# Performance work log

Hardware: AMD Instinct MI355X
Metric: run time of the kernel (lower is better)

## Reference

```python
import jax, jax.numpy as jnp
import numpy as np

B, L, Q = 2, 512, 512
E, W, D, H_NLM = 1024, 1024, 8, 32
NH = 16
HD = E // NH
SA, SO = 512, 1024
V = 8192
T = 6  # max_thought_step
SYN_H = 2048


def setup_inputs() -> dict:
    key = jax.random.key(0)
    ks = jax.random.split(key, 24)
    n = lambda k, shp, s=0.02: jax.random.normal(k, shp, dtype=jnp.float32) * s
    return {
        "x": jax.random.randint(ks[0], (B, L), 0, V),
        "num_output_q": Q,
        "emb": n(ks[1], (V, E)),
        "w_kv": n(ks[2], (E, E)),
        "w_q_sync": n(ks[3], (SA, E)),
        "wq": n(ks[4], (E, E)),
        "wk": n(ks[5], (E, E)),
        "wv": n(ks[6], (E, E)),
        "wo": n(ks[7], (E, E)),
        "ws1": n(ks[8], (E + W, SYN_H)),
        "bs1": jnp.zeros((SYN_H,), jnp.float32),
        "ws2": n(ks[9], (SYN_H, W)),
        "bs2": jnp.zeros((W,), jnp.float32),
        "nlm_w1": n(ks[10], (W, D, H_NLM), 0.1),
        "nlm_b1": jnp.zeros((W, H_NLM), jnp.float32),
        "nlm_w2": n(ks[11], (W, H_NLM), 0.1),
        "nlm_b2": jnp.zeros((W,), jnp.float32),
        "out_w": n(ks[12], (SO, V)),
        "out_b": jnp.zeros((V,), jnp.float32),
        "z_init": jax.random.normal(ks[13], (W,), dtype=jnp.float32),
        "pah_init": jax.random.normal(ks[14], (W, D), dtype=jnp.float32),
        "decay_a": jnp.zeros((SA,), jnp.float32),
        "decay_o": jnp.zeros((SO,), jnp.float32),
        "idx_la": jax.random.randint(ks[15], (SA,), 0, W),
        "idx_ra": jax.random.randint(ks[16], (SA,), 0, W),
        "idx_lo": jax.random.randint(ks[17], (SO,), 0, W),
        "idx_ro": jax.random.randint(ks[18], (SO,), 0, W),
    }


def _rope(xh, pos):
    # xh: [B, NH, S, HD]; rotate-half RoPE
    half = HD // 2
    inv = 1.0 / (10000.0 ** (jnp.arange(half, dtype=jnp.float32) / half))
    ang = pos.astype(jnp.float32)[:, None] * inv[None, :]  # [S, half]
    cos, sin = jnp.cos(ang), jnp.sin(ang)
    x1, x2 = xh[..., :half], xh[..., half:]
    return jnp.concatenate([x1 * cos - x2 * sin, x2 * cos + x1 * sin], axis=-1)


def _attention(q_in, kv, wq, wk, wv, wo):
    # causal cross-attention with RoPE on q and k
    Bq, Sq, _ = q_in.shape
    Sk = kv.shape[1]
    heads = lambda t: t.reshape(t.shape[0], t.shape[1], NH, HD).transpose(0, 2, 1, 3)
    qh = _rope(heads(q_in @ wq), jnp.arange(Sq))
    kh = _rope(heads(kv @ wk), jnp.arange(Sk))
    vh = heads(kv @ wv)
    scores = jnp.einsum('bhqd,bhkd->bhqk', qh, kh) / jnp.sqrt(jnp.float32(HD))
    i = jnp.arange(Sq)[:, None]
    j = jnp.arange(Sk)[None, :]
    scores = jnp.where(j <= i + (Sk - Sq), scores, jnp.float32(-1e30))
    out = jnp.einsum('bhqk,bhkd->bhqd', jax.nn.softmax(scores, axis=-1), vh)
    return out.transpose(0, 2, 1, 3).reshape(Bq, Sq, E) @ wo


def _compute_sync(hist, idx_l, idx_r, decay):
    # hist: list of [B,Q,W]; exponentially-decayed gather-multiply-reduce over time
    seq = jnp.stack(hist, axis=1)  # [B, Tn, Q, W]
    Tn = seq.shape[1]
    t_back = jnp.arange(Tn - 1, -1, -1, dtype=jnp.float32).reshape(1, Tn, 1, 1)
    ed = jnp.exp(-t_back * decay.reshape(1, 1, 1, -1))  # [1,Tn,1,S]
    sm = seq[..., idx_l] * ed * seq[..., idx_r]  # [B,Tn,Q,S]
    return sm.sum(axis=1) / jnp.sqrt(ed.sum(axis=1))  # [B,Q,S]


def reference(x, num_output_q, emb, w_kv, w_q_sync, wq, wk, wv, wo, ws1, bs1, ws2, bs2,
              nlm_w1, nlm_b1, nlm_w2, nlm_b2, out_w, out_b, z_init, pah_init,
              decay_a, decay_o, idx_la, idx_ra, idx_lo, idx_ro):
    emb_input = emb[x]                      # [B,L,E]
    kv = emb_input @ w_kv                   # [B,L,E]
    pah = jnp.broadcast_to(pah_init, (B, Q, W, D))
    z = jnp.broadcast_to(z_init, (B, Q, W))
    hist = [z]
    sync_a = _compute_sync(hist, idx_la, idx_ra, decay_a)
    outs = []
    for _ in range(T):
        q = sync_a @ w_q_sync               # [B,Q,E]
        attn_out = _attention(q, kv, wq, wk, wv, wo)
        pre = jnp.concatenate([attn_out, z], axis=-1)        # [B,Q,E+W]
        pre = jax.nn.gelu(pre @ ws1 + bs1) @ ws2 + bs2        # synapse -> [B,Q,W]
        pah = jnp.concatenate([pah[..., 1:], pre[..., None]], axis=-1)
        h = jax.nn.gelu(jnp.einsum('bqwd,wdh->bqwh', pah, nlm_w1) + nlm_b1)
        z = jnp.einsum('bqwh,wh->bqw', h, nlm_w2) + nlm_b2    # neuron-level model
        hist.append(z)
        sync_a = _compute_sync(hist, idx_la, idx_ra, decay_a)
        sync_o = _compute_sync(hist, idx_lo, idx_ro, decay_o)
        outs.append(sync_o @ out_w + out_b)                   # [B,Q,V]
    return jnp.stack(outs, axis=0)          # [T,B,Q,V]
```

## Files before the change

### kernel.cpp

```cpp
#include <hip/hip_runtime.h>

#define B_ 2
#define L_ 512
#define Q_ 512
#define E_ 1024
#define W_ 1024
#define D_ 8
#define H_ 32
#define NH_ 16
#define HD_ 64
#define SA_ 512
#define SO_ 1024
#define V_ 8192
#define T_ 6
#define SYNH_ 2048

#define BQ_ 1024
#define BL_ 1024

typedef __attribute__((ext_vector_type(8))) short bf16x8;
typedef __attribute__((ext_vector_type(4))) float f32x4;

__device__ __forceinline__ float gelu_f(float x) {
    const float c = 0.7978845608028654f;
    float x3 = x * x * x;
    return 0.5f * x * (1.0f + tanhf(c * (x + 0.044715f * x3)));
}

__device__ __forceinline__ unsigned short f2bf(float x) {
    unsigned int u = __float_as_uint(x);
    u += 0x7fffu + ((u >> 16) & 1u);
    return (unsigned short)(u >> 16);
}
__device__ __forceinline__ float bf2f(unsigned short h) {
    return __uint_as_float(((unsigned int)h) << 16);
}

__device__ __forceinline__ void gload16(const void* g, void* l) {
    __builtin_amdgcn_global_load_lds(
        (const __attribute__((address_space(1))) void*)g,
        (__attribute__((address_space(3))) void*)l, 16, 0, 0);
}

template<int TILE>
__global__ __launch_bounds__(256) void gemm_split_db(
    const unsigned short* __restrict__ Ah, const unsigned short* __restrict__ Al,
    const unsigned short* __restrict__ Bh, const unsigned short* __restrict__ Bl,
    float* __restrict__ C, unsigned short* __restrict__ CHp, unsigned short* __restrict__ CLp,
    int ldc, const float* __restrict__ bias,
    int M, int N, int K, int act)
{
    constexpr int FR = TILE / 32;
    constexpr int TS = TILE * 32;
    constexpr int NP = TS / 8 / 256;
    __shared__ unsigned short sAh[2][TS], sAl[2][TS], sBh[2][TS], sBl[2][TS];

    const int tid  = threadIdx.x;
    const int wave = tid >> 6;
    const int lane = tid & 63;
    const int r15 = lane & 15;
    const int r4  = lane >> 4;
    const int bm = blockIdx.y * TILE;
    const int bn = blockIdx.x * TILE;
    const int wm = (wave >> 1) * (TILE / 2);
    const int wn = (wave & 1) * (TILE / 2);

    f32x4 acc[FR][FR] = {};

    size_t goffA[NP], goffB[NP];
    int ldst[NP];
#pragma unroll
    for (int p2 = 0; p2 < NP; ++p2) {
        int ch = p2 * 256 + tid;
        int row = ch >> 2, c = ch & 3;
        int cs = c ^ ((row >> 1) & 3);
        goffA[p2] = (size_t)(bm + row) * K + cs * 8;
        goffB[p2] = (size_t)(bn + row) * K + cs * 8;
        ldst[p2] = (p2 * 256 + wave * 64) * 8;
    }

    const int nk = K / 32;
#pragma unroll
    for (int p2 = 0; p2 < NP; ++p2) {
        gload16(Ah + goffA[p2], &sAh[0][ldst[p2]]);
        gload16(Al + goffA[p2], &sAl[0][ldst[p2]]);
        gload16(Bh + goffB[p2], &sBh[0][ldst[p2]]);
        gload16(Bl + goffB[p2], &sBl[0][ldst[p2]]);
    }
    asm volatile("s_waitcnt vmcnt(0)" ::: "memory");
    __syncthreads();

    for (int t = 0; t < nk; ++t) {
        const int cur = t & 1;
        if (t + 1 < nk) {
            const size_t kadd = (size_t)(t + 1) * 32;
#pragma unroll
            for (int p2 = 0; p2 < NP; ++p2) {
                gload16(Ah + goffA[p2] + kadd, &sAh[cur ^ 1][ldst[p2]]);
                gload16(Al + goffA[p2] + kadd, &sAl[cur ^ 1][ldst[p2]]);
                gload16(Bh + goffB[p2] + kadd, &sBh[cur ^ 1][ldst[p2]]);
                gload16(Bl + goffB[p2] + kadd, &sBl[cur ^ 1][ldst[p2]]);
            }
        }
        bf16x8 afh[FR], afl[FR], bfh[FR], bfl[FR];
#pragma unroll
        for (int i = 0; i < FR; ++i) {
            const int row = wm + i * 16 + r15;
            const int off = row * 32 + (r4 ^ ((row >> 1) & 3)) * 8;
            afh[i] = *(const bf16x8*)(&sAh[cur][off]);
            afl[i] = *(const bf16x8*)(&sAl[cur][off]);
        }
#pragma unroll
        for (int j = 0; j < FR; ++j) {
            const int row = wn + j * 16 + r15;
            const int off = row * 32 + (r4 ^ ((row >> 1) & 3)) * 8;
            bfh[j] = *(const bf16x8*)(&sBh[cur][off]);
            bfl[j] = *(const bf16x8*)(&sBl[cur][off]);
        }
#pragma unroll
        for (int i = 0; i < FR; ++i)
#pragma unroll
            for (int j = 0; j < FR; ++j) {
                acc[i][j] = __builtin_amdgcn_mfma_f32_16x16x32_bf16(afh[i], bfh[j], acc[i][j], 0, 0, 0);
                acc[i][j] = __builtin_amdgcn_mfma_f32_16x16x32_bf16(afh[i], bfl[j], acc[i][j], 0, 0, 0);
                acc[i][j] = __builtin_amdgcn_mfma_f32_16x16x32_bf16(afl[i], bfh[j], acc[i][j], 0, 0, 0);
            }
        asm volatile("s_waitcnt vmcnt(0)" ::: "memory");
        __syncthreads();
    }

    const int crow0 = bm + wm + r4 * 4;
    const int ccol0 = bn + wn + r15;
#pragma unroll
    for (int i = 0; i < FR; ++i) {
#pragma unroll
        for (int j = 0; j < FR; ++j) {
            const int col = ccol0 + j * 16;
            const float bv = bias ? bias[col] : 0.0f;
#pragma unroll
            for (int r = 0; r < 4; ++r) {
                const int row = crow0 + i * 16 + r;
                float v = acc[i][j][r] + bv;
                if (act) v = gelu_f(v);
                const size_t o = (size_t)row * ldc + col;
                if (C) C[o] = v;
                if (CHp) {
                    unsigned short hh = f2bf(v);
                    CHp[o] = hh;
                    CLp[o] = f2bf(v - bf2f(hh));
                }
            }
        }
    }
}

__global__ __launch_bounds__(256) void attn_mfma(
    const unsigned short* __restrict__ qh_h, const unsigned short* __restrict__ qh_l,
    const unsigned short* __restrict__ kh_h, const unsigned short* __restrict__ kh_l,
    const unsigned short* __restrict__ vt_h, const unsigned short* __restrict__ vt_l,
    unsigned short* __restrict__ ctxH, unsigned short* __restrict__ ctxL)
{
    __shared__ unsigned short sKh[64 * 64], sKl[64 * 64];
    __shared__ unsigned short sVh[64 * 64], sVl[64 * 64];
    __shared__ unsigned short sPh[64 * 64], sPl[64 * 64];

    const int tid  = threadIdx.x;
    const int wave = tid >> 6;
    const int lane = tid & 63;
    const int r15 = lane & 15;
    const int r4  = lane >> 4;
    const int qt = blockIdx.x;
    const int h  = blockIdx.y;
    const int b  = blockIdx.z;
    const int bh = b * NH_ + h;
    const int qbase = qt * 64 + wave * 16;

    bf16x8 qa[2][2];
    {
        const unsigned short* qr_h = qh_h + ((size_t)bh * Q_ + qbase + r15) * HD_ + r4 * 8;
        const unsigned short* qr_l = qh_l + ((size_t)bh * Q_ + qbase + r15) * HD_ + r4 * 8;
        qa[0][0] = *(const bf16x8*)(qr_h);
        qa[1][0] = *(const bf16x8*)(qr_h + 32);
        qa[0][1] = *(const bf16x8*)(qr_l);
        qa[1][1] = *(const bf16x8*)(qr_l + 32);
    }

    f32x4 of[4] = {};
    float mrow[4] = {-1e30f, -1e30f, -1e30f, -1e30f};
    float lrow[4] = {};

    const int row0 = tid >> 3,        i70 = tid & 7;
    const int row1 = 32 + (tid >> 3), i71 = tid & 7;
    const int ko0 = row0 * 64 + ((i70 * 8) ^ ((row0 & 7) << 3));
    const int ko1 = row1 * 64 + ((i71 * 8) ^ ((row1 & 7) << 3));
    const size_t vo0 = (size_t)row0 * L_ + ((i70 * 8) ^ ((row0 & 7) << 3));
    const size_t vo1 = (size_t)row1 * L_ + ((i71 * 8) ^ ((row1 & 7) << 3));
    const int ld0 = wave * 512;
    const int ld1 = 2048 + wave * 512;

    const unsigned short* kb_h = kh_h + (size_t)bh * L_ * HD_;
    const unsigned short* kb_l = kh_l + (size_t)bh * L_ * HD_;
    const unsigned short* vb_h = vt_h + (size_t)bh * HD_ * L_;
    const unsigned short* vb_l = vt_l + (size_t)bh * HD_ * L_;

    for (int kt = 0; kt <= qt; ++kt) {
        gload16(kb_h + kt * 4096 + ko0, sKh + ld0);
        gload16(kb_h + kt * 4096 + ko1, sKh + ld1);
        gload16(kb_l + kt * 4096 + ko0, sKl + ld0);
        gload16(kb_l + kt * 4096 + ko1, sKl + ld1);
        gload16(vb_h + vo0 + kt * 64, sVh + ld0);
        gload16(vb_h + vo1 + kt * 64, sVh + ld1);
        gload16(vb_l + vo0 + kt * 64, sVl + ld0);
        gload16(vb_l + vo1 + kt * 64, sVl + ld1);
        asm volatile("s_waitcnt vmcnt(0)" ::: "memory");
        __syncthreads();

        f32x4 sf[4] = {};
#pragma unroll
        for (int ks = 0; ks < 2; ++ks) {
#pragma unroll
            for (int j = 0; j < 4; ++j) {
                const int kr = j * 16 + r15;
                const int off = kr * 64 + (((ks * 32 + r4 * 8)) ^ ((kr & 7) << 3));
                bf16x8 kfh = *(const bf16x8*)(sKh + off);
                bf16x8 kfl = *(const bf16x8*)(sKl + off);
                sf[j] = __builtin_amdgcn_mfma_f32_16x16x32_bf16(qa[ks][0], kfh, sf[j], 0, 0, 0);
                sf[j] = __builtin_amdgcn_mfma_f32_16x16x32_bf16(qa[ks][0], kfl, sf[j], 0, 0, 0);
                sf[j] = __builtin_amdgcn_mfma_f32_16x16x32_bf16(qa[ks][1], kfh, sf[j], 0, 0, 0);
            }
        }

        const bool diag = (kt == qt);
#pragma unroll
        for (int j = 0; j < 4; ++j)
#pragma unroll
            for (int r = 0; r < 4; ++r) {
                float s = sf[j][r] * 0.125f;
                if (diag) {
                    int kg = kt * 64 + j * 16 + r15;
                    int qg = qt * 64 + wave * 16 + r4 * 4 + r;
                    if (kg > qg) s = -1e30f;
                }
                sf[j][r] = s;
            }

        float pv[4][4];
#pragma unroll
        for (int r = 0; r < 4; ++r) {
            float mx = fmaxf(fmaxf(sf[0][r], sf[1][r]), fmaxf(sf[2][r], sf[3][r]));
#pragma unroll
            for (int d = 1; d < 16; d <<= 1) mx = fmaxf(mx, __shfl_xor(mx, d, 64));
            float mnew = fmaxf(mrow[r], mx);
            float corr = expf(mrow[r] - mnew);
            float rs = 0.0f;
#pragma unroll
            for (int j = 0; j < 4; ++j) {
                float pp = expf(sf[j][r] - mnew);
                pv[j][r] = pp;
                rs += pp;
            }
#pragma unroll
            for (int d = 1; d < 16; d <<= 1) rs += __shfl_xor(rs, d, 64);
            lrow[r] = lrow[r] * corr + rs;
            mrow[r] = mnew;
#pragma unroll
            for (int j = 0; j < 4; ++j) of[j][r] *= corr;
        }

#pragma unroll
        for (int j = 0; j < 4; ++j)
#pragma unroll
            for (int r = 0; r < 4; ++r) {
                const int prow = wave * 16 + r4 * 4 + r;
                const int pcol = j * 16 + r15;
                const int off = prow * 64 + (pcol ^ ((prow & 7) << 3));
                unsigned short ph = f2bf(pv[j][r]);
                sPh[off] = ph;
                sPl[off] = f2bf(pv[j][r] - bf2f(ph));
            }
        __syncthreads();

#pragma unroll
        for (int ks = 0; ks < 2; ++ks) {
            const int arow = wave * 16 + r15;
            const int aoff = arow * 64 + (((ks * 32 + r4 * 8)) ^ ((arow & 7) << 3));
            bf16x8 pah = *(const bf16x8*)(sPh + aoff);
            bf16x8 pal = *(const bf16x8*)(sPl + aoff);
#pragma unroll
            for (int j = 0; j < 4; ++j) {
                const int vrow = j * 16 + r15;
                const int voff = vrow * 64 + (((ks * 32 + r4 * 8)) ^ ((vrow & 7) << 3));
                bf16x8 vfh = *(const bf16x8*)(sVh + voff);
                bf16x8 vfl = *(const bf16x8*)(sVl + voff);
                of[j] = __builtin_amdgcn_mfma_f32_16x16x32_bf16(pah, vfh, of[j], 0, 0, 0);
                of[j] = __builtin_amdgcn_mfma_f32_16x16x32_bf16(pah, vfl, of[j], 0, 0, 0);
                of[j] = __builtin_amdgcn_mfma_f32_16x16x32_bf16(pal, vfh, of[j], 0, 0, 0);
            }
        }
        __syncthreads();
    }

    float linv[4];
#pragma unroll
    for (int r = 0; r < 4; ++r) linv[r] = 1.0f / lrow[r];
#pragma unroll
    for (int j = 0; j < 4; ++j)
#pragma unroll
        for (int r = 0; r < 4; ++r) {
            const int qg = qt * 64 + wave * 16 + r4 * 4 + r;
            const int dc = h * HD_ + j * 16 + r15;
            const size_t o = ((size_t)b * Q_ + qg) * E_ + dc;
            float v = of[j][r] * linv[r];
            unsigned short hh = f2bf(v);
            ctxH[o] = hh;
            ctxL[o] = f2bf(v - bf2f(hh));
        }
}

__global__ void cvt_split(const float* __restrict__ X,
                          unsigned short* __restrict__ H, unsigned short* __restrict__ L,
                          size_t n4)
{
    size_t i = (size_t)blockIdx.x * 256 + threadIdx.x;
    if (i >= n4) return;
    float4 v = ((const float4*)X)[i];
    ushort4 h, l;
    h.x = f2bf(v.x); l.x = f2bf(v.x - bf2f(h.x));
    h.y = f2bf(v.y); l.y = f2bf(v.y - bf2f(h.y));
    h.z = f2bf(v.z); l.z = f2bf(v.z - bf2f(h.z));
    h.w = f2bf(v.w); l.w = f2bf(v.w - bf2f(h.w));
    ((ushort4*)H)[i] = h;
    ((ushort4*)L)[i] = l;
}

__global__ __launch_bounds__(256) void cvt_split_T(
    const float* __restrict__ X, int R, int Cc,
    unsigned short* __restrict__ H, unsigned short* __restrict__ L)
{
    __shared__ float tile[32][33];
    const int rb = blockIdx.y * 32, cb = blockIdx.x * 32;
    const int tx = threadIdx.x & 31, ty = threadIdx.x >> 5;
#pragma unroll
    for (int r = 0; r < 32; r += 8)
        tile[ty + r][tx] = X[(size_t)(rb + ty + r) * Cc + cb + tx];
    __syncthreads();
#pragma unroll
    for (int r = 0; r < 32; r += 8) {
        float v = tile[tx][ty + r];
        unsigned short h = f2bf(v);
        unsigned short l = f2bf(v - bf2f(h));
        size_t o = (size_t)(cb + ty + r) * R + rb + tx;
        H[o] = h;
        L[o] = l;
    }
}

__global__ __launch_bounds__(256) void vtrans_split(
    const float* __restrict__ v_lin,
    unsigned short* __restrict__ H, unsigned short* __restrict__ L)
{
    __shared__ float tile[32][33];
    const int bh = blockIdx.z;
    const int b = bh >> 4, h = bh & 15;
    const int rb = blockIdx.y * 32;
    const int cb = blockIdx.x * 32;
    const int tx = threadIdx.x & 31, ty = threadIdx.x >> 5;
#pragma unroll
    for (int r = 0; r < 32; r += 8)
        tile[ty + r][tx] = v_lin[((size_t)b * L_ + rb + ty + r) * E_ + h * HD_ + cb + tx];
    __syncthreads();
#pragma unroll
    for (int r = 0; r < 32; r += 8) {
        float v = tile[tx][ty + r];
        unsigned short hh = f2bf(v);
        unsigned short ll = f2bf(v - bf2f(hh));
        size_t o = (size_t)bh * HD_ * L_ + (size_t)(cb + ty + r) * L_ + rb + tx;
        H[o] = hh;
        L[o] = ll;
    }
}

__global__ void gather_emb_split(const int* __restrict__ x, const float* __restrict__ emb,
                                 unsigned short* __restrict__ H, unsigned short* __restrict__ L) {
    size_t i = (size_t)blockIdx.x * 256 + threadIdx.x;
    const int e4n = E_ / 4;
    size_t row = i / e4n;
    int e4 = (int)(i % e4n);
    float4 v = *(((const float4*)(emb + (size_t)x[row] * E_)) + e4);
    ushort4 h, l;
    h.x = f2bf(v.x); l.x = f2bf(v.x - bf2f(h.x));
    h.y = f2bf(v.y); l.y = f2bf(v.y - bf2f(h.y));
    h.z = f2bf(v.z); l.z = f2bf(v.z - bf2f(h.z));
    h.w = f2bf(v.w); l.w = f2bf(v.w - bf2f(h.w));
    ((ushort4*)H)[i] = h;
    ((ushort4*)L)[i] = l;
}

__global__ void rope_heads_split(const float* __restrict__ lin,
                                 unsigned short* __restrict__ OH, unsigned short* __restrict__ OL,
                                 int S, int applyRope) {
    const int half = HD_ / 2;
    size_t idx = (size_t)blockIdx.x * 256 + threadIdx.x;
    size_t total = (size_t)B_ * S * NH_ * half;
    if (idx >= total) return;
    int d2 = (int)(idx % half);
    int h = (int)((idx / half) % NH_);
    int s = (int)((idx / ((size_t)half * NH_)) % S);
    int b = (int)(idx / ((size_t)half * NH_ * S));
    const float* src = lin + ((size_t)b * S + s) * E_ + h * HD_;
    float x1 = src[d2], x2 = src[d2 + half];
    float o1, o2;
    if (applyRope) {
        float invf = powf(10000.0f, -(float)d2 / (float)half);
        float ang = (float)s * invf;
        float c = cosf(ang), sn = sinf(ang);
        o1 = x1 * c - x2 * sn;
        o2 = x2 * c + x1 * sn;
    } else {
        o1 = x1; o2 = x2;
    }
    size_t dbase = (((size_t)b * NH_ + h) * S + s) * HD_;
    unsigned short h1s = f2bf(o1);
    unsigned short h2s = f2bf(o2);
    OH[dbase + d2] = h1s;
    OL[dbase + d2] = f2bf(o1 - bf2f(h1s));
    OH[dbase + d2 + half] = h2s;
    OL[dbase + d2 + half] = f2bf(o2 - bf2f(h2s));
}

__global__ void init_hist0(const float* __restrict__ z_init, float* __restrict__ hist0) {
    size_t i = (size_t)blockIdx.x * 256 + threadIdx.x;
    if (i >= (size_t)W_ * BQ_) return;
    hist0[i] = z_init[i / BQ_];
}

__global__ void init_pah(const float* __restrict__ pah_init, float* __restrict__ pah) {
    size_t i = (size_t)blockIdx.x * 256 + threadIdx.x;
    if (i >= (size_t)W_ * BQ_ * D_) return;
    int d = (int)(i % D_);
    int w = (int)(i / ((size_t)BQ_ * D_));
    pah[i] = pah_init[(size_t)w * D_ + d];
}

__global__ __launch_bounds__(256) void sync_kernel(
    const float* __restrict__ hist, int Tn,
    const int* __restrict__ idx_l, const int* __restrict__ idx_r,
    const float* __restrict__ decay,
    unsigned short* __restrict__ outH, unsigned short* __restrict__ outL, int S) {
    const int s = blockIdx.y;
    const int bq = blockIdx.x * 256 + threadIdx.x;
    const int wl = idx_l[s], wr = idx_r[s];
    const float dc = decay[s];
    float num = 0.0f, den = 0.0f;
    for (int t = 0; t < Tn; ++t) {
        float wgt = expf(-(float)(Tn - 1 - t) * dc);
        const float* hp = hist + (size_t)t * W_ * BQ_;
        num = fmaf(wgt * hp[(size_t)wl * BQ_ + bq], hp[(size_t)wr * BQ_ + bq], num);
        den += wgt;
    }
    float v = num * rsqrtf(den);
    unsigned short hh = f2bf(v);
    outH[(size_t)bq * S + s] = hh;
    outL[(size_t)bq * S + s] = f2bf(v - bf2f(hh));
}

__global__ void copy_z_cat_split(const float* __restrict__ z,
                                 unsigned short* __restrict__ catH,
                                 unsigned short* __restrict__ catL) {
    size_t i = (size_t)blockIdx.x * 256 + threadIdx.x;
    if (i >= (size_t)BQ_ * W_) return;
    size_t bq = i / W_;
    int w = (int)(i % W_);
    float v = z[(size_t)w * BQ_ + bq];
    unsigned short hh = f2bf(v);
    size_t o = bq * (E_ + W_) + E_ + w;
    catH[o] = hh;
    catL[o] = f2bf(v - bf2f(hh));
}

__global__ __launch_bounds__(256) void nlm_kernel(
    float* __restrict__ pah,
    const float* __restrict__ pre,
    const float* __restrict__ w1,
    const float* __restrict__ b1,
    const float* __restrict__ w2,
    const float* __restrict__ b2,
    float* __restrict__ zout)
{
    const int w = blockIdx.y;
    const int bq = blockIdx.x * 256 + threadIdx.x;
    const int tid = threadIdx.x;

    __shared__ float w1s[D_ * H_];
    __shared__ float b1s[H_];
    __shared__ float w2s[H_];
    w1s[tid] = w1[(size_t)w * D_ * H_ + tid];
    if (tid < H_) {
        b1s[tid] = b1[(size_t)w * H_ + tid];
        w2s[tid] = w2[(size_t)w * H_ + tid];
    }
    __syncthreads();

    float* pp = pah + ((size_t)w * BQ_ + bq) * D_;
    float4 lo = *(float4*)pp;
    float4 hi = *(float4*)(pp + 4);
    float p[D_];
    p[0] = lo.y; p[1] = lo.z; p[2] = lo.w;
    p[3] = hi.x; p[4] = hi.y; p[5] = hi.z; p[6] = hi.w;
    p[7] = pre[(size_t)bq * W_ + w];
    *(float4*)pp = make_float4(p[0], p[1], p[2], p[3]);
    *(float4*)(pp + 4) = make_float4(p[4], p[5], p[6], p[7]);

    float zacc = b2[w];
#pragma unroll
    for (int j = 0; j < H_; ++j) {
        float a = b1s[j];
#pragma unroll
        for (int d = 0; d < D_; ++d) a = fmaf(p[d], w1s[d * H_ + j], a);
        zacc = fmaf(gelu_f(a), w2s[j], zacc);
    }
    zout[(size_t)w * BQ_ + bq] = zacc;
}

static inline void gemm64(const unsigned short* Ah, const unsigned short* Al,
                          const unsigned short* Bh, const unsigned short* Bl,
                          float* C, unsigned short* CH, unsigned short* CL, int ldc,
                          const float* bias, int M, int N, int K, int act, hipStream_t s) {
    dim3 g(N / 64, M / 64);
    gemm_split_db<64><<<g, 256, 0, s>>>(Ah, Al, Bh, Bl, C, CH, CL, ldc, bias, M, N, K, act);
}
static inline void gemm128(const unsigned short* Ah, const unsigned short* Al,
                           const unsigned short* Bh, const unsigned short* Bl,
                           float* C, unsigned short* CH, unsigned short* CL, int ldc,
                           const float* bias, int M, int N, int K, int act, hipStream_t s) {
    dim3 g(N / 128, M / 128);
    gemm_split_db<128><<<g, 256, 0, s>>>(Ah, Al, Bh, Bl, C, CH, CL, ldc, bias, M, N, K, act);
}

static inline void launch_cvt(const float* X, unsigned short* H, unsigned short* L,
                              size_t n, hipStream_t s) {
    size_t n4 = n / 4;
    cvt_split<<<(unsigned)((n4 + 255) / 256), 256, 0, s>>>(X, H, L, n4);
}

static inline void launch_cvtT(const float* X, int R, int C,
                               unsigned short* H, unsigned short* L, hipStream_t s) {
    dim3 g(C / 32, R / 32);
    cvt_split_T<<<g, 256, 0, s>>>(X, R, C, H, L);
}

extern "C" void kernel_launch(void* const* d_in, const int* in_sizes, int n_in,
                              void* d_out, int out_size, void* d_ws, size_t ws_size,
                              hipStream_t stream) {
    const int*   x        = (const int*)d_in[0];
    const float* emb      = (const float*)d_in[2];
    const float* w_kv     = (const float*)d_in[3];
    const float* w_q_sync = (const float*)d_in[4];
    const float* wq       = (const float*)d_in[5];
    const float* wk       = (const float*)d_in[6];
    const float* wv       = (const float*)d_in[7];
    const float* wo       = (const float*)d_in[8];
    const float* ws1      = (const float*)d_in[9];
    const float* bs1      = (const float*)d_in[10];
    const float* ws2      = (const float*)d_in[11];
    const float* bs2      = (const float*)d_in[12];
    const float* nlm_w1   = (const float*)d_in[13];
    const float* nlm_b1   = (const float*)d_in[14];
    const float* nlm_w2   = (const float*)d_in[15];
    const float* nlm_b2   = (const float*)d_in[16];
    const float* out_w    = (const float*)d_in[17];
    const float* out_b    = (const float*)d_in[18];
    const float* z_init   = (const float*)d_in[19];
    const float* pah_init = (const float*)d_in[20];
    const float* decay_a  = (const float*)d_in[21];
    const float* decay_o  = (const float*)d_in[22];
    const int*   idx_la   = (const int*)d_in[23];
    const int*   idx_ra   = (const int*)d_in[24];
    const int*   idx_lo   = (const int*)d_in[25];
    const int*   idx_ro   = (const int*)d_in[26];

    float* out = (float*)d_out;

    const size_t BQ  = BQ_;
    const size_t BL  = BL_;
    const size_t BQW = BQ * W_;
    const size_t M1  = (size_t)1024 * 1024;

    float* p = (float*)d_ws;
    auto alloc = [&](size_t n) { float* r = p; p += n; return r; };
    auto alloc_us = [&](size_t n) { unsigned short* r = (unsigned short*)p; p += n / 2; return r; };

    float* k_lin  = alloc(M1);
    float* v_lin  = alloc(M1);
    float* pre    = alloc(M1);
    float* hist   = alloc((size_t)(T_ + 1) * BQW);
    float* pah    = alloc(BQW * D_);
    float* combined = alloc((size_t)SA_ * E_);

    float* q2 = k_lin;

    unsigned short* embS_h = alloc_us(M1);            unsigned short* embS_l = alloc_us(M1);
    unsigned short* wkvT_h = alloc_us(M1);            unsigned short* wkvT_l = alloc_us(M1);
    unsigned short* kvS_h  = alloc_us(M1);            unsigned short* kvS_l  = alloc_us(M1);
    unsigned short* wkT_h  = alloc_us(M1);            unsigned short* wkT_l  = alloc_us(M1);
    unsigned short* wvT_h  = alloc_us(M1);            unsigned short* wvT_l  = alloc_us(M1);
    unsigned short* wqsS_h = alloc_us(M1 / 2);        unsigned short* wqsS_l = alloc_us(M1 / 2);
    unsigned short* wqT_h  = alloc_us(M1);            unsigned short* wqT_l  = alloc_us(M1);
    unsigned short* combT_h = alloc_us(M1 / 2);       unsigned short* combT_l = alloc_us(M1 / 2);
    unsigned short* woT_h  = alloc_us(M1);            unsigned short* woT_l  = alloc_us(M1);
    unsigned short* ws1T_h = alloc_us(4 * M1);        unsigned short* ws1T_l = alloc_us(4 * M1);
    unsigned short* ws2T_h = alloc_us(2 * M1);        unsigned short* ws2T_l = alloc_us(2 * M1);
    unsigned short* outwT_h = alloc_us(8 * M1);       unsigned short* outwT_l = alloc_us(8 * M1);
    unsigned short* saS_h  = alloc_us(M1 / 2);        unsigned short* saS_l  = alloc_us(M1 / 2);
    unsigned short* ctxS_h = alloc_us(M1);            unsigned short* ctxS_l = alloc_us(M1);
    unsigned short* catS_h = alloc_us(2 * M1);        unsigned short* catS_l = alloc_us(2 * M1);
    unsigned short* h1S_h  = alloc_us(2 * M1);        unsigned short* h1S_l  = alloc_us(2 * M1);
    unsigned short* soS_h  = alloc_us(M1);            unsigned short* soS_l  = alloc_us(M1);
    unsigned short* qhS_h  = alloc_us(M1);            unsigned short* qhS_l  = alloc_us(M1);
    unsigned short* khS_h  = alloc_us(M1);            unsigned short* khS_l  = alloc_us(M1);
    unsigned short* vtS_h  = alloc_us(M1);            unsigned short* vtS_l  = alloc_us(M1);

    {
        size_t n = BL * (E_ / 4);
        gather_emb_split<<<(unsigned)((n + 255) / 256), 256, 0, stream>>>(x, emb, embS_h, embS_l);
    }
    launch_cvtT(w_kv, E_, E_, wkvT_h, wkvT_l, stream);
    gemm64(embS_h, embS_l, wkvT_h, wkvT_l, nullptr, kvS_h, kvS_l, E_, nullptr, (int)BL, E_, E_, 0, stream);
    launch_cvtT(wk, E_, E_, wkT_h, wkT_l, stream);
    launch_cvtT(wv, E_, E_, wvT_h, wvT_l, stream);
    gemm64(kvS_h, kvS_l, wkT_h, wkT_l, k_lin, nullptr, nullptr, E_, nullptr, (int)BL, E_, E_, 0, stream);
    gemm64(kvS_h, kvS_l, wvT_h, wvT_l, v_lin, nullptr, nullptr, E_, nullptr, (int)BL, E_, E_, 0, stream);
    {
        size_t n = (size_t)B_ * L_ * NH_ * (HD_ / 2);
        rope_heads_split<<<(unsigned)((n + 255) / 256), 256, 0, stream>>>(k_lin, khS_h, khS_l, L_, 1);
    }
    {
        dim3 g(HD_ / 32, L_ / 32, B_ * NH_);
        vtrans_split<<<g, 256, 0, stream>>>(v_lin, vtS_h, vtS_l);
    }
    launch_cvt(w_q_sync, wqsS_h, wqsS_l, (size_t)SA_ * E_, stream);
    launch_cvtT(wq, E_, E_, wqT_h, wqT_l, stream);
    gemm64(wqsS_h, wqsS_l, wqT_h, wqT_l, combined, nullptr, nullptr, E_, nullptr, SA_, E_, E_, 0, stream);
    launch_cvtT(combined, SA_, E_, combT_h, combT_l, stream);
    launch_cvtT(wo, E_, E_, woT_h, woT_l, stream);
    launch_cvtT(ws1, E_ + W_, SYNH_, ws1T_h, ws1T_l, stream);
    launch_cvtT(ws2, SYNH_, W_, ws2T_h, ws2T_l, stream);
    launch_cvtT(out_w, SO_, V_, outwT_h, outwT_l, stream);

    init_hist0<<<(unsigned)((BQW + 255) / 256), 256, 0, stream>>>(z_init, hist);
    init_pah<<<(unsigned)((BQW * D_ + 255) / 256), 256, 0, stream>>>(pah_init, pah);
    {
        dim3 g(BQ_ / 256, SA_);
        sync_kernel<<<g, 256, 0, stream>>>(hist, 1, idx_la, idx_ra, decay_a, saS_h, saS_l, SA_);
    }

    for (int t = 0; t < T_; ++t) {
        const float* z = hist + (size_t)t * BQW;

        gemm64(saS_h, saS_l, combT_h, combT_l, q2, nullptr, nullptr, E_, nullptr, (int)BQ, E_, SA_, 0, stream);
        {
            size_t n = (size_t)B_ * Q_ * NH_ * (HD_ / 2);
            rope_heads_split<<<(unsigned)((n + 255) / 256), 256, 0, stream>>>(q2, qhS_h, qhS_l, Q_, 1);
        }
        {
            dim3 g(Q_ / 64, NH_, B_);
            attn_mfma<<<g, 256, 0, stream>>>(qhS_h, qhS_l, khS_h, khS_l, vtS_h, vtS_l, ctxS_h, ctxS_l);
        }
        gemm64(ctxS_h, ctxS_l, woT_h, woT_l, nullptr, catS_h, catS_l, E_ + W_, nullptr, (int)BQ, E_, E_, 0, stream);
        copy_z_cat_split<<<(unsigned)((BQW + 255) / 256), 256, 0, stream>>>(z, catS_h, catS_l);

        gemm64(catS_h, catS_l, ws1T_h, ws1T_l, nullptr, h1S_h, h1S_l, SYNH_, bs1, (int)BQ, SYNH_, E_ + W_, 1, stream);
        gemm64(h1S_h, h1S_l, ws2T_h, ws2T_l, pre, nullptr, nullptr, W_, bs2, (int)BQ, W_, SYNH_, 0, stream);

        float* znext = hist + (size_t)(t + 1) * BQW;
        {
            dim3 g(BQ_ / 256, W_);
            nlm_kernel<<<g, 256, 0, stream>>>(pah, pre, nlm_w1, nlm_b1, nlm_w2, nlm_b2, znext);
        }

        int Tn = t + 2;
        if (t < T_ - 1) {
            dim3 g(BQ_ / 256, SA_);
            sync_kernel<<<g, 256, 0, stream>>>(hist, Tn, idx_la, idx_ra, decay_a, saS_h, saS_l, SA_);
        }
        {
            dim3 g(BQ_ / 256, SO_);
            sync_kernel<<<g, 256, 0, stream>>>(hist, Tn, idx_lo, idx_ro, decay_o, soS_h, soS_l, SO_);
        }

        float* out_t = out + (size_t)t * BQ * V_;
        gemm128(soS_h, soS_l, outwT_h, outwT_l, out_t, nullptr, nullptr, V_, out_b, (int)BQ, V_, SO_, 0, stream);
    }
}
```

Before: 2.101 ms.

## Fuse RoPE into q GEMM, triple-buffer 64 GEMM, merge sync kernels, drop attn LDS

Adds a triple-buffered 64x64 split-bf16 GEMM that keeps two K tiles in flight. It also makes a 128x128 GEMM variant whose epilogue applies RoPE and writes head-major split q directly, which removes the separate rope kernel and the fp32 intermediate. The two sync kernels per step are merged into one launch. The attention kernel stops staging K/V through LDS and reads fragments straight from global memory, which trades LDS reuse and barriers for more uncoalesced global/L2 traffic.

```diff
diff --git a/kernel.cpp b/kernel.cpp
--- a/kernel.cpp
+++ b/kernel.cpp
@@ -42,35 +42,129 @@
         (__attribute__((address_space(3))) void*)l, 16, 0, 0);
 }
 
-template<int TILE>
-__global__ __launch_bounds__(256) void gemm_split_db(
+__global__ __launch_bounds__(256) void gemm_split_deep(
     const unsigned short* __restrict__ Ah, const unsigned short* __restrict__ Al,
     const unsigned short* __restrict__ Bh, const unsigned short* __restrict__ Bl,
     float* __restrict__ C, unsigned short* __restrict__ CHp, unsigned short* __restrict__ CLp,
     int ldc, const float* __restrict__ bias,
     int M, int N, int K, int act)
 {
-    constexpr int FR = TILE / 32;
-    constexpr int TS = TILE * 32;
-    constexpr int NP = TS / 8 / 256;
-    __shared__ unsigned short sAh[2][TS], sAl[2][TS], sBh[2][TS], sBl[2][TS];
+    constexpr int TS = 64 * 32;
+    __shared__ unsigned short sAh[3][TS], sAl[3][TS], sBh[3][TS], sBl[3][TS];
 
     const int tid  = threadIdx.x;
     const int wave = tid >> 6;
     const int lane = tid & 63;
     const int r15 = lane & 15;
     const int r4  = lane >> 4;
-    const int bm = blockIdx.y * TILE;
-    const int bn = blockIdx.x * TILE;
-    const int wm = (wave >> 1) * (TILE / 2);
-    const int wn = (wave & 1) * (TILE / 2);
-
-    f32x4 acc[FR][FR] = {};
-
-    size_t goffA[NP], goffB[NP];
-    int ldst[NP];
-#pragma unroll
-    for (int p2 = 0; p2 < NP; ++p2) {
+    const int bm = blockIdx.y * 64;
+    const int bn = blockIdx.x * 64;
+    const int wm = (wave >> 1) * 32;
+    const int wn = (wave & 1) * 32;
+
+    f32x4 acc[2][2] = {};
+
+    const int row = tid >> 2, c = tid & 3;
+    const int cs = c ^ ((row >> 1) & 3);
+    const size_t goffA = (size_t)(bm + row) * K + cs * 8;
+    const size_t goffB = (size_t)(bn + row) * K + cs * 8;
+    const int ldst = wave * 512;
+
+    const int nk = K / 32;
+    auto issue = [&](int t, int bi) {
+        const size_t ka = (size_t)t * 32;
+        gload16(Ah + goffA + ka, &sAh[bi][ldst]);
+        gload16(Al + goffA + ka, &sAl[bi][ldst]);
+        gload16(Bh + goffB + ka, &sBh[bi][ldst]);
+        gload16(Bl + goffB + ka, &sBl[bi][ldst]);
+    };
+    issue(0, 0);
+    if (nk > 1) issue(1, 1);
+
+    for (int t = 0; t < nk; ++t) {
+        if (t + 1 < nk) asm volatile("s_waitcnt vmcnt(4)" ::: "memory");
+        else            asm volatile("s_waitcnt vmcnt(0)" ::: "memory");
+        __syncthreads();
+        if (t + 2 < nk) issue(t + 2, (t + 2) % 3);
+
+        const int bi = t % 3;
+        bf16x8 afh[2], afl[2], bfh[2], bfl[2];
+#pragma unroll
+        for (int i = 0; i < 2; ++i) {
+            const int rr = wm + i * 16 + r15;
+            const int off = rr * 32 + (r4 ^ ((rr >> 1) & 3)) * 8;
+            afh[i] = *(const bf16x8*)(&sAh[bi][off]);
+            afl[i] = *(const bf16x8*)(&sAl[bi][off]);
+        }
+#pragma unroll
+        for (int j = 0; j < 2; ++j) {
+            const int rr = wn + j * 16 + r15;
+            const int off = rr * 32 + (r4 ^ ((rr >> 1) & 3)) * 8;
+            bfh[j] = *(const bf16x8*)(&sBh[bi][off]);
+            bfl[j] = *(const bf16x8*)(&sBl[bi][off]);
+        }
+#pragma unroll
+        for (int i = 0; i < 2; ++i)
+#pragma unroll
+            for (int j = 0; j < 2; ++j) {
+                acc[i][j] = __builtin_amdgcn_mfma_f32_16x16x32_bf16(afh[i], bfh[j], acc[i][j], 0, 0, 0);
+                acc[i][j] = __builtin_amdgcn_mfma_f32_16x16x32_bf16(afh[i], bfl[j], acc[i][j], 0, 0, 0);
+                acc[i][j] = __builtin_amdgcn_mfma_f32_16x16x32_bf16(afl[i], bfh[j], acc[i][j], 0, 0, 0);
+            }
+    }
+
+    const int crow0 = bm + wm + r4 * 4;
+    const int ccol0 = bn + wn + r15;
+#pragma unroll
+    for (int i = 0; i < 2; ++i) {
+#pragma unroll
+        for (int j = 0; j < 2; ++j) {
+            const int col = ccol0 + j * 16;
+            const float bv = bias ? bias[col] : 0.0f;
+#pragma unroll
+            for (int r = 0; r < 4; ++r) {
+                const int rw = crow0 + i * 16 + r;
+                float v = acc[i][j][r] + bv;
+                if (act) v = gelu_f(v);
+                const size_t o = (size_t)rw * ldc + col;
+                if (C) C[o] = v;
+                if (CHp) {
+                    unsigned short hh = f2bf(v);
+                    CHp[o] = hh;
+                    CLp[o] = f2bf(v - bf2f(hh));
+                }
+            }
+        }
+    }
+}
+
+template<int EPI>
+__global__ __launch_bounds__(256) void gemm_split_128(
+    const unsigned short* __restrict__ Ah, const unsigned short* __restrict__ Al,
+    const unsigned short* __restrict__ Bh, const unsigned short* __restrict__ Bl,
+    float* __restrict__ C, unsigned short* __restrict__ CHp, unsigned short* __restrict__ CLp,
+    int ldc, const float* __restrict__ bias,
+    int M, int N, int K, int act)
+{
+    constexpr int TS = 128 * 32;
+    __shared__ unsigned short sAh[2][TS], sAl[2][TS], sBh[2][TS], sBl[2][TS];
+
+    const int tid  = threadIdx.x;
+    const int wave = tid >> 6;
+    const int lane = tid & 63;
+    const int r15 = lane & 15;
+    const int r4  = lane >> 4;
+    const int bm = blockIdx.y * 128;
+    const int bn = blockIdx.x * 128;
+    const int wm = (wave >> 1) * 64;
+    const int wn = (wave & 1) * 64;
+
+    f32x4 acc[4][4] = {};
+
+    size_t goffA[2], goffB[2];
+    int ldst[2];
+#pragma unroll
+    for (int p2 = 0; p2 < 2; ++p2) {
         int ch = p2 * 256 + tid;
         int row = ch >> 2, c = ch & 3;
         int cs = c ^ ((row >> 1) & 3);
@@ -81,7 +175,7 @@
 
     const int nk = K / 32;
 #pragma unroll
-    for (int p2 = 0; p2 < NP; ++p2) {
+    for (int p2 = 0; p2 < 2; ++p2) {
         gload16(Ah + goffA[p2], &sAh[0][ldst[p2]]);
         gload16(Al + goffA[p2], &sAl[0][ldst[p2]]);
         gload16(Bh + goffB[p2], &sBh[0][ldst[p2]]);
@@ -95,32 +189,32 @@
         if (t + 1 < nk) {
             const size_t kadd = (size_t)(t + 1) * 32;
 #pragma unroll
-            for (int p2 = 0; p2 < NP; ++p2) {
+            for (int p2 = 0; p2 < 2; ++p2) {
                 gload16(Ah + goffA[p2] + kadd, &sAh[cur ^ 1][ldst[p2]]);
                 gload16(Al + goffA[p2] + kadd, &sAl[cur ^ 1][ldst[p2]]);
                 gload16(Bh + goffB[p2] + kadd, &sBh[cur ^ 1][ldst[p2]]);
                 gload16(Bl + goffB[p2] + kadd, &sBl[cur ^ 1][ldst[p2]]);
             }
         }
-        bf16x8 afh[FR], afl[FR], bfh[FR], bfl[FR];
-#pragma unroll
-        for (int i = 0; i < FR; ++i) {
-            const int row = wm + i * 16 + r15;
-            const int off = row * 32 + (r4 ^ ((row >> 1) & 3)) * 8;
+        bf16x8 afh[4], afl[4], bfh[4], bfl[4];
+#pragma unroll
+        for (int i = 0; i < 4; ++i) {
+            const int rr = wm + i * 16 + r15;
+            const int off = rr * 32 + (r4 ^ ((rr >> 1) & 3)) * 8;
             afh[i] = *(const bf16x8*)(&sAh[cur][off]);
             afl[i] = *(const bf16x8*)(&sAl[cur][off]);
         }
 #pragma unroll
-        for (int j = 0; j < FR; ++j) {
-            const int row = wn + j * 16 + r15;
-            const int off = row * 32 + (r4 ^ ((row >> 1) & 3)) * 8;
+        for (int j = 0; j < 4; ++j) {
+            const int rr = wn + j * 16 + r15;
+            const int off = rr * 32 + (r4 ^ ((rr >> 1) & 3)) * 8;
             bfh[j] = *(const bf16x8*)(&sBh[cur][off]);
             bfl[j] = *(const bf16x8*)(&sBl[cur][off]);
         }
 #pragma unroll
-        for (int i = 0; i < FR; ++i)
-#pragma unroll
-            for (int j = 0; j < FR; ++j) {
+        for (int i = 0; i < 4; ++i)
+#pragma unroll
+            for (int j = 0; j < 4; ++j) {
                 acc[i][j] = __builtin_amdgcn_mfma_f32_16x16x32_bf16(afh[i], bfh[j], acc[i][j], 0, 0, 0);
                 acc[i][j] = __builtin_amdgcn_mfma_f32_16x16x32_bf16(afh[i], bfl[j], acc[i][j], 0, 0, 0);
                 acc[i][j] = __builtin_amdgcn_mfma_f32_16x16x32_bf16(afl[i], bfh[j], acc[i][j], 0, 0, 0);
@@ -129,25 +223,55 @@
         __syncthreads();
     }
 
-    const int crow0 = bm + wm + r4 * 4;
-    const int ccol0 = bn + wn + r15;
-#pragma unroll
-    for (int i = 0; i < FR; ++i) {
-#pragma unroll
-        for (int j = 0; j < FR; ++j) {
-            const int col = ccol0 + j * 16;
-            const float bv = bias ? bias[col] : 0.0f;
+    if constexpr (EPI == 0) {
+        const int crow0 = bm + wm + r4 * 4;
+        const int ccol0 = bn + wn + r15;
+#pragma unroll
+        for (int i = 0; i < 4; ++i) {
+#pragma unroll
+            for (int j = 0; j < 4; ++j) {
+                const int col = ccol0 + j * 16;
+                const float bv = bias ? bias[col] : 0.0f;
+#pragma unroll
+                for (int r = 0; r < 4; ++r) {
+                    const int rw = crow0 + i * 16 + r;
+                    float v = acc[i][j][r] + bv;
+                    if (act) v = gelu_f(v);
+                    const size_t o = (size_t)rw * ldc + col;
+                    if (C) C[o] = v;
+                    if (CHp) {
+                        unsigned short hh = f2bf(v);
+                        CHp[o] = hh;
+                        CLp[o] = f2bf(v - bf2f(hh));
+                    }
+                }
+            }
+        }
+    } else {
+        const int crow0 = bm + wm + r4 * 4;
+#pragma unroll
+        for (int i = 0; i < 4; ++i) {
 #pragma unroll
             for (int r = 0; r < 4; ++r) {
-                const int row = crow0 + i * 16 + r;
-                float v = acc[i][j][r] + bv;
-                if (act) v = gelu_f(v);
-                const size_t o = (size_t)row * ldc + col;
-                if (C) C[o] = v;
-                if (CHp) {
-                    unsigned short hh = f2bf(v);
-                    CHp[o] = hh;
-                    CLp[o] = f2bf(v - bf2f(hh));
+                const int rw = crow0 + i * 16 + r;
+                const int b = rw >> 9, q = rw & 511;
+#pragma unroll
+                for (int j = 0; j < 2; ++j) {
+                    const int col = bn + wn + j * 16 + r15;
+                    const int hh = col >> 6;
+                    const int d2 = col & 31;
+                    float x1 = acc[i][j][r], x2 = acc[i][j + 2][r];
+                    float invf = powf(10000.0f, -(float)d2 / 32.0f);
+                    float ang = (float)q * invf;
+                    float cc = cosf(ang), sn = sinf(ang);
+                    float o1 = x1 * cc - x2 * sn;
+                    float o2 = x2 * cc + x1 * sn;
+                    size_t dbase = (((size_t)b * NH_ + hh) * Q_ + q) * HD_;
+                    unsigned short u1 = f2bf(o1), u2 = f2bf(o2);
+                    CHp[dbase + d2] = u1;
+                    CLp[dbase + d2] = f2bf(o1 - bf2f(u1));
+                    CHp[dbase + d2 + 32] = u2;
+                    CLp[dbase + d2 + 32] = f2bf(o2 - bf2f(u2));
                 }
             }
         }
@@ -160,8 +284,6 @@
     const unsigned short* __restrict__ vt_h, const unsigned short* __restrict__ vt_l,
     unsigned short* __restrict__ ctxH, unsigned short* __restrict__ ctxL)
 {
-    __shared__ unsigned short sKh[64 * 64], sKl[64 * 64];
-    __shared__ unsigned short sVh[64 * 64], sVl[64 * 64];
     __shared__ unsigned short sPh[64 * 64], sPl[64 * 64];
 
     const int tid  = threadIdx.x;
@@ -189,41 +311,20 @@
     float mrow[4] = {-1e30f, -1e30f, -1e30f, -1e30f};
     float lrow[4] = {};
 
-    const int row0 = tid >> 3,        i70 = tid & 7;
-    const int row1 = 32 + (tid >> 3), i71 = tid & 7;
-    const int ko0 = row0 * 64 + ((i70 * 8) ^ ((row0 & 7) << 3));
-    const int ko1 = row1 * 64 + ((i71 * 8) ^ ((row1 & 7) << 3));
-    const size_t vo0 = (size_t)row0 * L_ + ((i70 * 8) ^ ((row0 & 7) << 3));
-    const size_t vo1 = (size_t)row1 * L_ + ((i71 * 8) ^ ((row1 & 7) << 3));
-    const int ld0 = wave * 512;
-    const int ld1 = 2048 + wave * 512;
-
     const unsigned short* kb_h = kh_h + (size_t)bh * L_ * HD_;
     const unsigned short* kb_l = kh_l + (size_t)bh * L_ * HD_;
     const unsigned short* vb_h = vt_h + (size_t)bh * HD_ * L_;
     const unsigned short* vb_l = vt_l + (size_t)bh * HD_ * L_;
 
     for (int kt = 0; kt <= qt; ++kt) {
-        gload16(kb_h + kt * 4096 + ko0, sKh + ld0);
-        gload16(kb_h + kt * 4096 + ko1, sKh + ld1);
-        gload16(kb_l + kt * 4096 + ko0, sKl + ld0);
-        gload16(kb_l + kt * 4096 + ko1, sKl + ld1);
-        gload16(vb_h + vo0 + kt * 64, sVh + ld0);
-        gload16(vb_h + vo1 + kt * 64, sVh + ld1);
-        gload16(vb_l + vo0 + kt * 64, sVl + ld0);
-        gload16(vb_l + vo1 + kt * 64, sVl + ld1);
-        asm volatile("s_waitcnt vmcnt(0)" ::: "memory");
-        __syncthreads();
-
         f32x4 sf[4] = {};
 #pragma unroll
         for (int ks = 0; ks < 2; ++ks) {
 #pragma unroll
             for (int j = 0; j < 4; ++j) {
-                const int kr = j * 16 + r15;
-                const int off = kr * 64 + (((ks * 32 + r4 * 8)) ^ ((kr & 7) << 3));
-                bf16x8 kfh = *(const bf16x8*)(sKh + off);
-                bf16x8 kfl = *(const bf16x8*)(sKl + off);
+                const size_t ko = (size_t)(kt * 64 + j * 16 + r15) * HD_ + ks * 32 + r4 * 8;
+                bf16x8 kfh = *(const bf16x8*)(kb_h + ko);
+                bf16x8 kfl = *(const bf16x8*)(kb_l + ko);
                 sf[j] = __builtin_amdgcn_mfma_f32_16x16x32_bf16(qa[ks][0], kfh, sf[j], 0, 0, 0);
                 sf[j] = __builtin_amdgcn_mfma_f32_16x16x32_bf16(qa[ks][0], kfl, sf[j], 0, 0, 0);
                 sf[j] = __builtin_amdgcn_mfma_f32_16x16x32_bf16(qa[ks][1], kfh, sf[j], 0, 0, 0);
@@ -288,10 +389,9 @@
             bf16x8 pal = *(const bf16x8*)(sPl + aoff);
 #pragma unroll
             for (int j = 0; j < 4; ++j) {
-                const int vrow = j * 16 + r15;
-                const int voff = vrow * 64 + (((ks * 32 + r4 * 8)) ^ ((vrow & 7) << 3));
-                bf16x8 vfh = *(const bf16x8*)(sVh + voff);
-                bf16x8 vfl = *(const bf16x8*)(sVl + voff);
+                const size_t vo = (size_t)(j * 16 + r15) * L_ + kt * 64 + ks * 32 + r4 * 8;
+                bf16x8 vfh = *(const bf16x8*)(vb_h + vo);
+                bf16x8 vfl = *(const bf16x8*)(vb_l + vo);
                 of[j] = __builtin_amdgcn_mfma_f32_16x16x32_bf16(pah, vfh, of[j], 0, 0, 0);
                 of[j] = __builtin_amdgcn_mfma_f32_16x16x32_bf16(pah, vfl, of[j], 0, 0, 0);
                 of[j] = __builtin_amdgcn_mfma_f32_16x16x32_bf16(pal, vfh, of[j], 0, 0, 0);
@@ -464,6 +564,39 @@
     outL[(size_t)bq * S + s] = f2bf(v - bf2f(hh));
 }
 
+__global__ __launch_bounds__(256) void sync_fused(
+    const float* __restrict__ hist, int Tn,
+    const int* __restrict__ idx_la, const int* __restrict__ idx_ra,
+    const float* __restrict__ decay_a,
+    unsigned short* __restrict__ saH, unsigned short* __restrict__ saL,
+    const int* __restrict__ idx_lo, const int* __restrict__ idx_ro,
+    const float* __restrict__ decay_o,
+    unsigned short* __restrict__ soH, unsigned short* __restrict__ soL,
+    int doA)
+{
+    const int s0 = blockIdx.y;
+    const bool isA = doA && (s0 < SA_);
+    const int s = isA ? s0 : (s0 - (doA ? SA_ : 0));
+    const int S = isA ? SA_ : SO_;
+    const int wl = isA ? idx_la[s] : idx_lo[s];
+    const int wr = isA ? idx_ra[s] : idx_ro[s];
+    const float dc = isA ? decay_a[s] : decay_o[s];
+    unsigned short* oh = isA ? saH : soH;
+    unsigned short* ol = isA ? saL : soL;
+    const int bq = blockIdx.x * 256 + threadIdx.x;
+    float num = 0.0f, den = 0.0f;
+    for (int t = 0; t < Tn; ++t) {
+        float wgt = expf(-(float)(Tn - 1 - t) * dc);
+        const float* hp = hist + (size_t)t * W_ * BQ_;
+        num = fmaf(wgt * hp[(size_t)wl * BQ_ + bq], hp[(size_t)wr * BQ_ + bq], num);
+        den += wgt;
+    }
+    float v = num * rsqrtf(den);
+    unsigned short hh = f2bf(v);
+    oh[(size_t)bq * S + s] = hh;
+    ol[(size_t)bq * S + s] = f2bf(v - bf2f(hh));
+}
+
 __global__ void copy_z_cat_split(const float* __restrict__ z,
                                  unsigned short* __restrict__ catH,
                                  unsigned short* __restrict__ catL) {
@@ -527,14 +660,21 @@
                           float* C, unsigned short* CH, unsigned short* CL, int ldc,
                           const float* bias, int M, int N, int K, int act, hipStream_t s) {
     dim3 g(N / 64, M / 64);
-    gemm_split_db<64><<<g, 256, 0, s>>>(Ah, Al, Bh, Bl, C, CH, CL, ldc, bias, M, N, K, act);
+    gemm_split_deep<<<g, 256, 0, s>>>(Ah, Al, Bh, Bl, C, CH, CL, ldc, bias, M, N, K, act);
 }
 static inline void gemm128(const unsigned short* Ah, const unsigned short* Al,
                            const unsigned short* Bh, const unsigned short* Bl,
                            float* C, unsigned short* CH, unsigned short* CL, int ldc,
                            const float* bias, int M, int N, int K, int act, hipStream_t s) {
     dim3 g(N / 128, M / 128);
-    gemm_split_db<128><<<g, 256, 0, s>>>(Ah, Al, Bh, Bl, C, CH, CL, ldc, bias, M, N, K, act);
+    gemm_split_128<0><<<g, 256, 0, s>>>(Ah, Al, Bh, Bl, C, CH, CL, ldc, bias, M, N, K, act);
+}
+static inline void gemm128_rope(const unsigned short* Ah, const unsigned short* Al,
+                                const unsigned short* Bh, const unsigned short* Bl,
+                                unsigned short* QH, unsigned short* QL,
+                                int M, int N, int K, hipStream_t s) {
+    dim3 g(N / 128, M / 128);
+    gemm_split_128<1><<<g, 256, 0, s>>>(Ah, Al, Bh, Bl, nullptr, QH, QL, 0, nullptr, M, N, K, 0);
 }
 
 static inline void launch_cvt(const float* X, unsigned short* H, unsigned short* L,
@@ -597,8 +737,6 @@
     float* pah    = alloc(BQW * D_);
     float* combined = alloc((size_t)SA_ * E_);
 
-    float* q2 = k_lin;
-
     unsigned short* embS_h = alloc_us(M1);            unsigned short* embS_l = alloc_us(M1);
     unsigned short* wkvT_h = alloc_us(M1);            unsigned short* wkvT_l = alloc_us(M1);
     unsigned short* kvS_h  = alloc_us(M1);            unsigned short* kvS_l  = alloc_us(M1);
@@ -657,11 +795,7 @@
     for (int t = 0; t < T_; ++t) {
         const float* z = hist + (size_t)t * BQW;
 
-        gemm64(saS_h, saS_l, combT_h, combT_l, q2, nullptr, nullptr, E_, nullptr, (int)BQ, E_, SA_, 0, stream);
-        {
-            size_t n = (size_t)B_ * Q_ * NH_ * (HD_ / 2);
-            rope_heads_split<<<(unsigned)((n + 255) / 256), 256, 0, stream>>>(q2, qhS_h, qhS_l, Q_, 1);
-        }
+        gemm128_rope(saS_h, saS_l, combT_h, combT_l, qhS_h, qhS_l, (int)BQ, E_, SA_, stream);
         {
             dim3 g(Q_ / 64, NH_, B_);
             attn_mfma<<<g, 256, 0, stream>>>(qhS_h, qhS_l, khS_h, khS_l, vtS_h, vtS_l, ctxS_h, ctxS_l);
@@ -679,13 +813,11 @@
         }
 
         int Tn = t + 2;
-        if (t < T_ - 1) {
-            dim3 g(BQ_ / 256, SA_);
-            sync_kernel<<<g, 256, 0, stream>>>(hist, Tn, idx_la, idx_ra, decay_a, saS_h, saS_l, SA_);
-        }
+        int doA = (t < T_ - 1) ? 1 : 0;
         {
-            dim3 g(BQ_ / 256, SO_);
-            sync_kernel<<<g, 256, 0, stream>>>(hist, Tn, idx_lo, idx_ro, decay_o, soS_h, soS_l, SO_);
+            dim3 g(BQ_ / 256, doA ? (SA_ + SO_) : SO_);
+            sync_fused<<<g, 256, 0, stream>>>(hist, Tn, idx_la, idx_ra, decay_a, saS_h, saS_l,
+                                              idx_lo, idx_ro, decay_o, soS_h, soS_l, doA);
         }
 
         float* out_t = out + (size_t)t * BQ * V_;
```

Result: slower. 2.551 ms (+21.4%).
